# Performance work log

Measured on AMD Instinct MI355X. Metric: run time of the kernel, lower is better.

The kernel has to match this reference:

```python
import jax, jax.numpy as jnp
import numpy as np

K = 15  # window_size


def setup_inputs() -> dict:
    key = jax.random.key(0)
    k1, k2, k3, k4 = jax.random.split(key, 4)
    x = jax.random.normal(k1, (8, 256, 240, 240), dtype=jnp.float32)
    wq = jax.random.normal(k2, (144, 256), dtype=jnp.float32) * (1.0 / np.sqrt(256))
    wk = jax.random.normal(k3, (144, 256), dtype=jnp.float32) * (1.0 / np.sqrt(256))
    wproj = jax.random.normal(k4, (256, 256), dtype=jnp.float32) * (1.0 / np.sqrt(256))
    return {"x": x, "wq": wq, "wk": wk, "wproj": wproj}


def _pnlm(x, wq, wk, wproj):
    b, c, h, w = x.shape
    ph, pw = (-h) % K, (-w) % K
    if ph or pw:
        x_pad = jnp.pad(x, ((0, 0), (0, 0), (0, ph), (0, pw)), mode='reflect')
    else:
        x_pad = x
    H, W = x_pad.shape[2], x_pad.shape[3]
    nh, nw = H // K, W // K
    N = K * K  # tokens per window
    # blockify: (B,C,H,W) -> (B*nh*nw, C, N)
    blocks = (x_pad.reshape(b, c, nh, K, nw, K)
              .transpose(0, 2, 4, 1, 3, 5)
              .reshape(b * nh * nw, c, N))
    q = jnp.einsum('ec,bcn->bne', wq, blocks)   # (B', N, E)
    km = jnp.einsum('ec,bcm->bem', wk, blocks)  # (B', E, N)
    att = jnp.einsum('bne,bem->bnm', q, km)     # (B', N, N)
    scale = 1.0 / jnp.sqrt(jnp.asarray(q.shape[-1], dtype=att.dtype))
    att = jax.nn.softmax(att * scale, axis=-1)
    y = jnp.einsum('bnm,bcm->bcn', att, blocks)  # att @ V, V = blocks^T
    y = jnp.einsum('oc,bcn->bon', wproj, y)      # 1x1 proj_out
    # unblockify: (B', C, N) -> (B, C, H, W)
    y = (y.reshape(b, nh, nw, c, K, K)
         .transpose(0, 3, 1, 4, 2, 5)
         .reshape(b, c, H, W))
    y = y[:, :, :h, :w]
    return x + y


def reference(x, wq, wk, wproj):
    return _pnlm(x, wq, wk, wproj)
```

## Files before the change

### kernel.cpp

```cpp
#include <hip/hip_runtime.h>


typedef __bf16 bf16x8 __attribute__((ext_vector_type(8)));
typedef float  f32x4  __attribute__((ext_vector_type(4)));

#define MFMA(a,b,c) __builtin_amdgcn_mfma_f32_16x16x32_bf16((a),(b),(c),0,0,0)

#define QK_ROW 320
#define KL_STRIDE 168
#define XBB_ROW 240

__device__ __forceinline__ unsigned short f2bf(float f){
  union { float f; unsigned int u; } v; v.f = f;
  unsigned int r = v.u + 0x7FFFu + ((v.u >> 16) & 1u);
  return (unsigned short)(r >> 16);
}
__device__ __forceinline__ float bf2f(unsigned short u){
  union { unsigned int u; float f; } v; v.u = ((unsigned int)u) << 16;
  return v.f;
}
__device__ __forceinline__ int swz(int row, int col){
  return row*256 + ((((col >> 3) ^ (row & 7)) << 3) | (col & 7));
}
__device__ __forceinline__ int swzC(int row, int col){
  return row*256 + (col ^ ((((row >> 3) ^ row) & 7) << 3));
}
__device__ __forceinline__ bf16x8 ld_frag_lds(const unsigned short* p, int idx){
  uint4 v = *(const uint4*)(p + idx);
  return __builtin_bit_cast(bf16x8, v);
}
__device__ __forceinline__ bf16x8 ld_frag_b(const void* p){
  uint4 v = *(const uint4*)(p);
  return __builtin_bit_cast(bf16x8, v);
}

__device__ __forceinline__ void repack_frag(const unsigned int* plo, const unsigned int* phi,
                                            uint4* outf, int lane){
  const int nn = lane & 15, hh = lane >> 4;
  const int sla = nn + 32*(hh & 1);
  const int slb = sla + 16;
  const bool up = hh >= 2;
  #pragma unroll
  for (int k = 0; k < 8; ++k){
    unsigned int a0 = (unsigned int)__shfl((int)plo[2*k],   sla);
    unsigned int a1 = (unsigned int)__shfl((int)plo[2*k+1], sla);
    unsigned int b0 = (unsigned int)__shfl((int)phi[2*k],   sla);
    unsigned int b1 = (unsigned int)__shfl((int)phi[2*k+1], sla);
    unsigned int c0 = (unsigned int)__shfl((int)plo[2*k],   slb);
    unsigned int c1 = (unsigned int)__shfl((int)plo[2*k+1], slb);
    unsigned int d0 = (unsigned int)__shfl((int)phi[2*k],   slb);
    unsigned int d1 = (unsigned int)__shfl((int)phi[2*k+1], slb);
    outf[k] = make_uint4(up?a1:a0, up?b1:b0, up?c1:c0, up?d1:d0);
  }
}

__global__ __launch_bounds__(256) void k_w(
    const float* __restrict__ wq, const float* __restrict__ wk,
    const float* __restrict__ wproj,
    unsigned short* __restrict__ wqb, unsigned short* __restrict__ wkb,
    unsigned short* __restrict__ wpb)
{
  int i = blockIdx.x*256 + threadIdx.x;
  if (i < 20480){
    int e = i >> 7, c = (i & 127)*2;
    unsigned int v = 0;
    if (e < 144) v = (unsigned int)f2bf(wq[e*256+c]) | ((unsigned int)f2bf(wq[e*256+c+1]) << 16);
    *(unsigned int*)(wqb + (size_t)i*2) = v;
  } else if (i < 40960){
    int j = i - 20480;
    int e = j >> 7, c = (j & 127)*2;
    unsigned int v = 0;
    if (e < 144) v = (unsigned int)f2bf(wk[e*256+c]) | ((unsigned int)f2bf(wk[e*256+c+1]) << 16);
    *(unsigned int*)(wkb + (size_t)j*2) = v;
  } else if (i < 73728){
    int l = i - 40960;
    int o = l >> 7, c = (l & 127)*2;
    *(unsigned int*)(wpb + (size_t)l*2) =
        (unsigned int)f2bf(wproj[o*256+c]) | ((unsigned int)f2bf(wproj[o*256+c+1]) << 16);
  }
}

__global__ __launch_bounds__(256) void k_xb(
    const float* __restrict__ x, unsigned short* __restrict__ xbb)
{
  __shared__ unsigned short xs[8*15*240];
  const int wg = blockIdx.x;
  const int cg = wg & 31;
  const int th = (wg >> 5) & 15;
  const int b  = wg >> 9;
  const int tid = threadIdx.x;

  const float* xb = x + ((size_t)b*256 + cg*8)*57600 + th*15*240;
  for (int i = tid; i < 8*15*120; i += 256){
    int c = i / 1800;
    int rem = i - c*1800;
    int r = rem / 120, p2 = rem - r*120;
    float2 v = *(const float2*)(xb + (size_t)c*57600 + r*240 + p2*2);
    *(unsigned int*)(&xs[(c*15 + r)*240 + p2*2]) =
        (unsigned int)f2bf(v.x) | ((unsigned int)f2bf(v.y) << 16);
  }
  __syncthreads();

  for (int i = tid; i < 8*16*30; i += 256){
    int c = i / 480;
    int rem = i - c*480;
    int tw = rem / 30, ch = rem - tw*30;
    union { unsigned short u16[8]; uint4 u4; } pk;
    #pragma unroll
    for (int j = 0; j < 8; ++j){
      int m = ch*8 + j;
      int r = m / 15, s = m - r*15;
      pk.u16[j] = (m <= 224) ? xs[(c*15 + r)*240 + tw*15 + s] : (unsigned short)0;
    }
    *(uint4*)(xbb + ((size_t)(b*256 + th*16 + tw)*256 + cg*8 + c)*XBB_ROW + ch*8) = pk.u4;
  }
}

__global__ __launch_bounds__(512) void k_qkb(
    const unsigned short* __restrict__ xbb,
    const unsigned short* __restrict__ wqb, const unsigned short* __restrict__ wkb,
    unsigned short* __restrict__ qkws)
{
  __shared__ __align__(16) unsigned short S[32768];
  unsigned short* xt  = S;
  unsigned short* wqs = S;
  unsigned short* wks = S + 8192;
  const int wg = blockIdx.x;
  const int b  = wg >> 8;
  const int th = (wg >> 4) & 15, tw = wg & 15;
  const int h0 = th*15, w0 = tw*15;
  const int tid = threadIdx.x;
  const int lane = tid & 63, wave = tid >> 6;
  const int col  = lane & 15, hi = lane >> 4;
  const unsigned short* xbw = xbb + (size_t)wg * (256*XBB_ROW);

  bf16x8 af[2][8];
  #pragma unroll 1
  for (int half = 0; half < 2; ++half){
    if (half) __syncthreads();
    for (int i = tid; i < 256*16; i += 512){
      int c = i >> 4, m8 = i & 15;
      int m = half*128 + m8*8;
      if (m + 8 <= 240){
        uint4 v = *(const uint4*)(xbw + (size_t)c*XBB_ROW + m);
        const unsigned short* pv = (const unsigned short*)&v;
        #pragma unroll
        for (int j = 0; j < 8; ++j)
          xt[swzC(m8*8 + j, c)] = pv[j];
      }
    }
    __syncthreads();
    const int rloc = wave*16 + col;
    if (half == 0){
      #pragma unroll
      for (int k = 0; k < 8; ++k)
        af[0][k] = ld_frag_lds(xt, swzC(rloc, k*32 + hi*8));
    } else {
      #pragma unroll
      for (int k = 0; k < 8; ++k)
        af[1][k] = ld_frag_lds(xt, swzC(rloc, k*32 + hi*8));
    }
  }
  __syncthreads();

  #pragma unroll 1
  for (int eg = 0; eg < 5; ++eg){
    if (eg) __syncthreads();
    for (int i = tid; i < 32*32; i += 512){
      int e_l = i >> 5, c8 = (i & 31)*8;
      size_t off = (size_t)(eg*32 + e_l)*256 + c8;
      *(uint4*)(&wqs[swz(e_l, c8)]) = *(const uint4*)(wqb + off);
      *(uint4*)(&wks[swz(e_l, c8)]) = *(const uint4*)(wkb + off);
    }
    __syncthreads();
    #pragma unroll
    for (int h2 = 0; h2 < 2; ++h2){
      const int t = h2*8 + wave;
      if (t < 15){
        #pragma unroll
        for (int et = 0; et < 2; ++et){
          f32x4 aq = {0.f,0.f,0.f,0.f}, ak = {0.f,0.f,0.f,0.f};
          const int el = et*16 + col;
          #pragma unroll
          for (int k = 0; k < 8; ++k){
            int idx = swz(el, k*32 + hi*8);
            bf16x8 bq = ld_frag_lds(wqs, idx);
            bf16x8 bk = ld_frag_lds(wks, idx);
            aq = MFMA(af[h2][k], bq, aq);
            ak = MFMA(af[h2][k], bk, ak);
          }
          const int e_out = eg*32 + et*16 + col;
          #pragma unroll
          for (int jj = 0; jj < 4; ++jj){
            int m_px = t*16 + hi*4 + jj;
            if (m_px <= 224){
              int hw = (h0 + m_px/15)*240 + w0 + m_px%15;
              size_t row = ((size_t)b*57600 + hw)*QK_ROW;
              qkws[row + e_out]       = f2bf(aq[jj]);
              qkws[row + 160 + e_out] = f2bf(ak[jj]);
            }
          }
        }
      }
    }
  }
}

__global__ __launch_bounds__(512,4) void k_attn_b(
    const unsigned short* __restrict__ xbb, const unsigned short* __restrict__ wpb,
    const unsigned short* __restrict__ qkws, float* __restrict__ out)
{
  __shared__ __align__(16) unsigned short S[40960];
  unsigned short* kl = S;
  unsigned short* xl = S;
  unsigned short* wl = S + 32768;
  unsigned int*  hwp = (unsigned int*)(S + 40320);
  const int wg = blockIdx.x;
  const int b  = wg >> 8;
  const int th = (wg >> 4) & 15, tw = wg & 15;
  const int h0 = th*15, w0 = tw*15;
  const int tid = threadIdx.x;
  const int lane = tid & 63, wave = tid >> 6;
  const int col  = lane & 15, hi = lane >> 4;
  const size_t obase = (size_t)b * 256 * 57600;
  const unsigned short* qkb = qkws + (size_t)b * 57600 * QK_ROW;
  const unsigned short* xbw = xbb + (size_t)wg * (256*XBB_ROW);

  if (tid < 240){
    int ms = tid <= 224 ? tid : 224;
    hwp[tid] = (unsigned int)((h0 + ms/15)*240 + w0 + ms%15);
  }
  __syncthreads();

  for (int i = tid; i < 240*20; i += 512){
    int m = i / 20, eb = i - m*20;
    *(uint4*)(&kl[m*KL_STRIDE + eb*8]) =
        *(const uint4*)(qkb + (size_t)hwp[m]*QK_ROW + 160 + eb*8);
  }
  __syncthreads();

  uint4 attf[2][8];
  #pragma unroll
  for (int slot = 0; slot < 2; ++slot){
    const int nt = wave + slot*8;
    if (nt < 15){
      const int n  = nt*16 + col;
      const int na = n <= 224 ? n : 224;
      const unsigned short* qrow = qkb + (size_t)hwp[na]*QK_ROW;
      bf16x8 qf[5];
      #pragma unroll
      for (int c = 0; c < 5; ++c)
        qf[c] = ld_frag_b(qrow + c*32 + hi*8);
      f32x4 at[15];
      #pragma unroll
      for (int T = 0; T < 15; ++T){
        f32x4 acc = {0.f,0.f,0.f,0.f};
        #pragma unroll
        for (int c = 0; c < 5; ++c){
          bf16x8 kf = ld_frag_lds(kl, (T*16 + col)*KL_STRIDE + c*32 + hi*8);
          acc = MFMA(kf, qf[c], acc);
        }
        at[T] = acc;
      }
      const float sc = 0.12022458674074695f;
      float M = -3.0e38f;
      #pragma unroll
      for (int T = 0; T < 15; ++T){
        #pragma unroll
        for (int jj = 0; jj < 4; ++jj){
          int m = T*16 + hi*4 + jj;
          if (m <= 224) M = fmaxf(M, at[T][jj]*sc);
        }
      }
      M = fmaxf(M, __shfl_xor(M, 16));
      M = fmaxf(M, __shfl_xor(M, 32));
      float Ssum = 0.f;
      #pragma unroll
      for (int T = 0; T < 15; ++T){
        #pragma unroll
        for (int jj = 0; jj < 4; ++jj){
          int m = T*16 + hi*4 + jj;
          float v = (m <= 224) ? exp2f(at[T][jj]*sc - M) : 0.f;
          at[T][jj] = v; Ssum += v;
        }
      }
      Ssum += __shfl_xor(Ssum, 16);
      Ssum += __shfl_xor(Ssum, 32);
      const float inv = 1.0f / Ssum;
      unsigned int plo[16], phi[16];
      #pragma unroll
      for (int T = 0; T < 15; ++T){
        plo[T] = (unsigned int)f2bf(at[T][0]*inv) | ((unsigned int)f2bf(at[T][1]*inv) << 16);
        phi[T] = (unsigned int)f2bf(at[T][2]*inv) | ((unsigned int)f2bf(at[T][3]*inv) << 16);
      }
      plo[15] = 0u; phi[15] = 0u;
      repack_frag(plo, phi, attf[slot], lane);
    }
  }

  int pixs[2];
  #pragma unroll
  for (int slot = 0; slot < 2; ++slot){
    const int n = (wave + slot*8)*16 + col;
    pixs[slot] = (n <= 224) ? (int)hwp[n] : -1;
  }

  unsigned int ylo[2][16], yhi[2][16];
  #pragma unroll
  for (int half = 0; half < 2; ++half){
    __syncthreads();
    for (int i = tid; i < 128*32; i += 512){
      int c = i >> 5, m8 = i & 31;
      uint4 v = make_uint4(0u,0u,0u,0u);
      if (m8 < 30)
        v = *(const uint4*)(xbw + (size_t)(half*128 + c)*XBB_ROW + m8*8);
      *(uint4*)(&xl[swz(c, m8*8)]) = v;
    }
    __syncthreads();
    #pragma unroll
    for (int slot = 0; slot < 2; ++slot){
      const int nt = wave + slot*8;
      if (nt < 15){
        #pragma unroll
        for (int ct = 0; ct < 8; ++ct){
          f32x4 acc = {0.f,0.f,0.f,0.f};
          #pragma unroll
          for (int k = 0; k < 8; ++k){
            bf16x8 xf = ld_frag_lds(xl, swz(ct*16 + col, k*32 + hi*8));
            acc = MFMA(xf, __builtin_bit_cast(bf16x8, attf[slot][k]), acc);
          }
          ylo[slot][half*8 + ct] = (unsigned int)f2bf(acc[0]) | ((unsigned int)f2bf(acc[1]) << 16);
          yhi[slot][half*8 + ct] = (unsigned int)f2bf(acc[2]) | ((unsigned int)f2bf(acc[3]) << 16);
        }
      }
    }
  }

  uint4 y1f[2][8];
  #pragma unroll
  for (int slot = 0; slot < 2; ++slot){
    const int nt = wave + slot*8;
    if (nt < 15)
      repack_frag(ylo[slot], yhi[slot], y1f[slot], lane);
  }

  #pragma unroll 1
  for (int oe = 0; oe < 8; ++oe){
    __syncthreads();
    for (int i = tid; i < 32*32; i += 512){
      int olr = i >> 5, c8 = (i & 31)*8;
      *(uint4*)(&wl[swz(olr, c8)]) =
          *(const uint4*)(wpb + (size_t)(oe*32 + olr)*256 + c8);
    }
    __syncthreads();
    #pragma unroll
    for (int ot = 0; ot < 2; ++ot){
      bf16x8 awf[8];
      const int olr = ot*16 + col;
      #pragma unroll
      for (int k = 0; k < 8; ++k)
        awf[k] = ld_frag_lds(wl, swz(olr, k*32 + hi*8));
      #pragma unroll
      for (int slot = 0; slot < 2; ++slot){
        const int nt = wave + slot*8;
        if (nt < 15){
          f32x4 y2 = {0.f,0.f,0.f,0.f};
          #pragma unroll
          for (int k = 0; k < 8; ++k)
            y2 = MFMA(awf[k], __builtin_bit_cast(bf16x8, y1f[slot][k]), y2);
          const int n = nt*16 + col;
          if (n <= 224){
            const size_t pix = (size_t)pixs[slot];
            #pragma unroll
            for (int jj = 0; jj < 4; ++jj){
              int o = oe*32 + ot*16 + hi*4 + jj;
              float xr = bf2f(xbw[(size_t)o*XBB_ROW + n]);
              out[obase + (size_t)o*57600 + pix] = y2[jj] + xr;
            }
          }
        }
      }
    }
  }
}

__global__ __launch_bounds__(512) void k_qk(
    const float* __restrict__ x, const float* __restrict__ wq,
    const float* __restrict__ wk,
    unsigned short* __restrict__ qkws)
{
  __shared__ __align__(16) unsigned short S[32768];
  unsigned short* xt  = S;
  unsigned short* wqs = S;
  unsigned short* wks = S + 8192;
  const int wg  = blockIdx.x;
  const int b   = wg / 450;
  const int hw0 = (wg % 450) * 128;
  const int tid = threadIdx.x;
  const int lane = tid & 63, wave = tid >> 6;
  const int col  = lane & 15, hi = lane >> 4;

  {
    const float* xb = x + (size_t)b * 256 * 57600 + hw0;
    const int hw_l = tid & 127;
    #pragma unroll 4
    for (int i = 0; i < 32; ++i){
      int c = ((tid >> 7) * 32 + i) * 2;
      float f0 = xb[(size_t)c     * 57600 + hw_l];
      float f1 = xb[(size_t)(c+1) * 57600 + hw_l];
      *(unsigned int*)(&xt[swz(hw_l, c)]) =
          (unsigned int)f2bf(f0) | ((unsigned int)f2bf(f1) << 16);
    }
  }
  __syncthreads();

  bf16x8 af[8];
  const int arow = wave*16 + col;
  #pragma unroll
  for (int k = 0; k < 8; ++k)
    af[k] = ld_frag_lds(xt, swz(arow, k*32 + hi*8));

  const size_t orow_base = (size_t)b*57600 + hw0 + wave*16;

  for (int eg = 0; eg < 5; ++eg){
    __syncthreads();
    for (int i = 0; i < 8; ++i){
      int idx = tid + i*512;
      int e_l = idx >> 7, c = (idx & 127) * 2;
      int e = eg*32 + e_l;
      float2 vq = make_float2(0.f,0.f), vk = make_float2(0.f,0.f);
      if (e < 144){
        vq = *(const float2*)(wq + (size_t)e*256 + c);
        vk = *(const float2*)(wk + (size_t)e*256 + c);
      }
      *(unsigned int*)(&wqs[swz(e_l, c)]) =
          (unsigned int)f2bf(vq.x) | ((unsigned int)f2bf(vq.y) << 16);
      *(unsigned int*)(&wks[swz(e_l, c)]) =
          (unsigned int)f2bf(vk.x) | ((unsigned int)f2bf(vk.y) << 16);
    }
    __syncthreads();
    #pragma unroll
    for (int etl = 0; etl < 2; ++etl){
      f32x4 aq = {0.f,0.f,0.f,0.f}, ak = {0.f,0.f,0.f,0.f};
      const int el = etl*16 + col;
      #pragma unroll
      for (int k = 0; k < 8; ++k){
        int idx = swz(el, k*32 + hi*8);
        bf16x8 bq = ld_frag_lds(wqs, idx);
        bf16x8 bk = ld_frag_lds(wks, idx);
        aq = MFMA(af[k], bq, aq);
        ak = MFMA(af[k], bk, ak);
      }
      const int e_out = eg*32 + etl*16 + col;
      #pragma unroll
      for (int jj = 0; jj < 4; ++jj){
        size_t row = orow_base + hi*4 + jj;
        qkws[row*QK_ROW + e_out]       = f2bf(aq[jj]);
        qkws[row*QK_ROW + 160 + e_out] = f2bf(ak[jj]);
      }
    }
  }
}

__global__ __launch_bounds__(512,4) void k_attn_s(
    const float* __restrict__ x, const float* __restrict__ wproj,
    const unsigned short* __restrict__ qkws, float* __restrict__ out)
{
  __shared__ __align__(16) unsigned short S[40320 + 480];
  unsigned short* kl = S;
  unsigned short* xl = S;
  unsigned short* wl = S + 32768;
  unsigned int*  hwp = (unsigned int*)(S + 40320);
  const int wg = blockIdx.x;
  const int b  = wg >> 8;
  const int th = (wg >> 4) & 15, tw = wg & 15;
  const int h0 = th*15, w0 = tw*15;
  const int tid = threadIdx.x;
  const int lane = tid & 63, wave = tid >> 6;
  const int col  = lane & 15, hi = lane >> 4;
  const size_t xbase = (size_t)b * 256 * 57600;
  const unsigned short* qkb = qkws + (size_t)b * 57600 * QK_ROW;

  if (tid < 240){
    int ms = tid <= 224 ? tid : 224;
    hwp[tid] = (unsigned int)((h0 + ms/15)*240 + w0 + ms%15);
  }
  __syncthreads();

  for (int i = tid; i < 240*20; i += 512){
    int m = i / 20, eb = i - m*20;
    *(uint4*)(&kl[m*KL_STRIDE + eb*8]) =
        *(const uint4*)(qkb + (size_t)hwp[m]*QK_ROW + 160 + eb*8);
  }
  __syncthreads();

  uint4 attf[2][8];
  #pragma unroll
  for (int slot = 0; slot < 2; ++slot){
    const int nt = wave + slot*8;
    if (nt < 15){
      const int n  = nt*16 + col;
      const int na = n <= 224 ? n : 224;
      const unsigned short* qrow = qkb + (size_t)hwp[na]*QK_ROW;
      bf16x8 qf[5];
      #pragma unroll
      for (int c = 0; c < 5; ++c)
        qf[c] = ld_frag_b(qrow + c*32 + hi*8);
      f32x4 at[15];
      #pragma unroll
      for (int T = 0; T < 15; ++T){
        f32x4 acc = {0.f,0.f,0.f,0.f};
        #pragma unroll
        for (int c = 0; c < 5; ++c){
          bf16x8 kf = ld_frag_lds(kl, (T*16 + col)*KL_STRIDE + c*32 + hi*8);
          acc = MFMA(kf, qf[c], acc);
        }
        at[T] = acc;
      }
      const float sc = 0.12022458674074695f;
      float M = -3.0e38f;
      #pragma unroll
      for (int T = 0; T < 15; ++T){
        #pragma unroll
        for (int jj = 0; jj < 4; ++jj){
          int m = T*16 + hi*4 + jj;
          if (m <= 224) M = fmaxf(M, at[T][jj]*sc);
        }
      }
      M = fmaxf(M, __shfl_xor(M, 16));
      M = fmaxf(M, __shfl_xor(M, 32));
      float Ssum = 0.f;
      #pragma unroll
      for (int T = 0; T < 15; ++T){
        #pragma unroll
        for (int jj = 0; jj < 4; ++jj){
          int m = T*16 + hi*4 + jj;
          float v = (m <= 224) ? exp2f(at[T][jj]*sc - M) : 0.f;
          at[T][jj] = v; Ssum += v;
        }
      }
      Ssum += __shfl_xor(Ssum, 16);
      Ssum += __shfl_xor(Ssum, 32);
      const float inv = 1.0f / Ssum;
      unsigned int plo[16], phi[16];
      #pragma unroll
      for (int T = 0; T < 15; ++T){
        plo[T] = (unsigned int)f2bf(at[T][0]*inv) | ((unsigned int)f2bf(at[T][1]*inv) << 16);
        phi[T] = (unsigned int)f2bf(at[T][2]*inv) | ((unsigned int)f2bf(at[T][3]*inv) << 16);
      }
      plo[15] = 0u; phi[15] = 0u;
      repack_frag(plo, phi, attf[slot], lane);
    }
  }

  unsigned int ylo[2][16], yhi[2][16];
  #pragma unroll
  for (int half = 0; half < 2; ++half){
    __syncthreads();
    for (int i = tid; i < 128*128; i += 512){
      int c = i >> 7, m = (i & 127)*2;
      int m0 = m <= 224 ? m : 224;
      float f0 = (m     <= 224) ? x[xbase + (size_t)(half*128 + c)*57600 + hwp[m0]]   : 0.f;
      float f1 = (m + 1 <= 224) ? x[xbase + (size_t)(half*128 + c)*57600 + hwp[m0+1]] : 0.f;
      *(unsigned int*)(&xl[swz(c, m)]) =
          (unsigned int)f2bf(f0) | ((unsigned int)f2bf(f1) << 16);
    }
    __syncthreads();
    #pragma unroll
    for (int slot = 0; slot < 2; ++slot){
      const int nt = wave + slot*8;
      if (nt < 15){
        #pragma unroll
        for (int ct = 0; ct < 8; ++ct){
          f32x4 acc = {0.f,0.f,0.f,0.f};
          #pragma unroll
          for (int k = 0; k < 8; ++k){
            bf16x8 xf = ld_frag_lds(xl, swz(ct*16 + col, k*32 + hi*8));
            acc = MFMA(xf, __builtin_bit_cast(bf16x8, attf[slot][k]), acc);
          }
          ylo[slot][half*8 + ct] = (unsigned int)f2bf(acc[0]) | ((unsigned int)f2bf(acc[1]) << 16);
          yhi[slot][half*8 + ct] = (unsigned int)f2bf(acc[2]) | ((unsigned int)f2bf(acc[3]) << 16);
        }
      }
    }
  }

  uint4 y1f[2][8];
  #pragma unroll
  for (int slot = 0; slot < 2; ++slot){
    const int nt = wave + slot*8;
    if (nt < 15)
      repack_frag(ylo[slot], yhi[slot], y1f[slot], lane);
  }

  #pragma unroll 1
  for (int oe = 0; oe < 16; ++oe){
    __syncthreads();
    for (int i = tid; i < 16*128; i += 512){
      int olr = i >> 7, c = (i & 127)*2;
      const float* wr = wproj + (size_t)(oe*16 + olr)*256 + c;
      *(unsigned int*)(&wl[swz(olr, c)]) =
          (unsigned int)f2bf(wr[0]) | ((unsigned int)f2bf(wr[1]) << 16);
    }
    __syncthreads();
    bf16x8 awf[8];
    #pragma unroll
    for (int k = 0; k < 8; ++k)
      awf[k] = ld_frag_lds(wl, swz(col, k*32 + hi*8));
    #pragma unroll
    for (int slot = 0; slot < 2; ++slot){
      const int nt = wave + slot*8;
      if (nt < 15){
        f32x4 y2 = {0.f,0.f,0.f,0.f};
        #pragma unroll
        for (int k = 0; k < 8; ++k)
          y2 = MFMA(awf[k], __builtin_bit_cast(bf16x8, y1f[slot][k]), y2);
        const int n = nt*16 + col;
        if (n <= 224){
          const size_t pix = hwp[n];
          #pragma unroll
          for (int jj = 0; jj < 4; ++jj){
            int o = oe*16 + hi*4 + jj;
            const size_t idx = xbase + (size_t)o*57600 + pix;
            out[idx] = y2[jj] + x[idx];
          }
        }
      }
    }
  }
}

extern "C" void kernel_launch(void* const* d_in, const int* in_sizes, int n_in,
                              void* d_out, int out_size, void* d_ws, size_t ws_size,
                              hipStream_t stream)
{
  const float* x     = (const float*)d_in[0];
  const float* wq    = (const float*)d_in[1];
  const float* wk    = (const float*)d_in[2];
  const float* wproj = (const float*)d_in[3];
  float* out = (float*)d_out;
  (void)in_sizes; (void)n_in; (void)out_size;

  const size_t QKWS_B = (size_t)8*57600*QK_ROW*2;
  const size_t XBB_B  = (size_t)8*256*256*XBB_ROW*2;
  const size_t WB_ALL = (size_t)(160*256 + 160*256 + 256*256)*2;
  unsigned short* qkws = (unsigned short*)d_ws;

  if (ws_size >= QKWS_B + XBB_B + WB_ALL){
    unsigned short* xbb = (unsigned short*)((char*)d_ws + QKWS_B);
    unsigned short* wqb = (unsigned short*)((char*)d_ws + QKWS_B + XBB_B);
    unsigned short* wkb = wqb + 160*256;
    unsigned short* wpb = wkb + 160*256;
    k_w     <<<dim3(288),  dim3(256), 0, stream>>>(wq, wk, wproj, wqb, wkb, wpb);
    k_xb    <<<dim3(4096), dim3(256), 0, stream>>>(x, xbb);
    k_qkb   <<<dim3(2048), dim3(512), 0, stream>>>(xbb, wqb, wkb, qkws);
    k_attn_b<<<dim3(2048), dim3(512), 0, stream>>>(xbb, wpb, qkws, out);
  } else {
    k_qk    <<<dim3(3600), dim3(512), 0, stream>>>(x, wq, wk, qkws);
    k_attn_s<<<dim3(2048), dim3(512), 0, stream>>>(x, wproj, qkws, out);
  }
}
```

Baseline: 954.5 us.

## Fuse QK projection and windowed attention kernels into one launch

Merges the Q/K projection kernel and the attention+projection kernel into a single kernel, so each workgroup computes its window's Q/K and then immediately runs attention on it. Intermediate Q/K still goes through global memory, but it is read back by the same workgroup while likely still in L2, and one launch plus its tail are removed. The output projection loop now stages 64 weight rows per iteration instead of 32, halving the barriers. Risk: the stricter launch bounds applied to the QK phase may increase register pressure or spills.

Result: no change. 945.7 us, median of 2 (-0.9%).

```diff
diff --git a/kernel.cpp b/kernel.cpp
--- a/kernel.cpp
+++ b/kernel.cpp
@@ -116,15 +116,20 @@
   }
 }
 
-__global__ __launch_bounds__(512) void k_qkb(
+__global__ __launch_bounds__(512,4) void k_fused(
     const unsigned short* __restrict__ xbb,
     const unsigned short* __restrict__ wqb, const unsigned short* __restrict__ wkb,
-    unsigned short* __restrict__ qkws)
+    const unsigned short* __restrict__ wpb,
+    unsigned short* __restrict__ qkws, float* __restrict__ out)
 {
-  __shared__ __align__(16) unsigned short S[32768];
+  __shared__ __align__(16) unsigned short S[40960];
   unsigned short* xt  = S;
   unsigned short* wqs = S;
   unsigned short* wks = S + 8192;
+  unsigned short* kl  = S;
+  unsigned short* xl  = S;
+  unsigned short* wl  = S;
+  unsigned int*  hwp  = (unsigned int*)(S + 40320);
   const int wg = blockIdx.x;
   const int b  = wg >> 8;
   const int th = (wg >> 4) & 15, tw = wg & 15;
@@ -132,7 +137,14 @@
   const int tid = threadIdx.x;
   const int lane = tid & 63, wave = tid >> 6;
   const int col  = lane & 15, hi = lane >> 4;
+  const size_t obase = (size_t)b * 256 * 57600;
+  const unsigned short* qkb = qkws + (size_t)b * 57600 * QK_ROW;
   const unsigned short* xbw = xbb + (size_t)wg * (256*XBB_ROW);
+
+  if (tid < 240){
+    int ms = tid <= 224 ? tid : 224;
+    hwp[tid] = (unsigned int)((h0 + ms/15)*240 + w0 + ms%15);
+  }
 
   bf16x8 af[2][8];
   #pragma unroll 1
@@ -204,32 +216,6 @@
       }
     }
   }
-}
-
-__global__ __launch_bounds__(512,4) void k_attn_b(
-    const unsigned short* __restrict__ xbb, const unsigned short* __restrict__ wpb,
-    const unsigned short* __restrict__ qkws, float* __restrict__ out)
-{
-  __shared__ __align__(16) unsigned short S[40960];
-  unsigned short* kl = S;
-  unsigned short* xl = S;
-  unsigned short* wl = S + 32768;
-  unsigned int*  hwp = (unsigned int*)(S + 40320);
-  const int wg = blockIdx.x;
-  const int b  = wg >> 8;
-  const int th = (wg >> 4) & 15, tw = wg & 15;
-  const int h0 = th*15, w0 = tw*15;
-  const int tid = threadIdx.x;
-  const int lane = tid & 63, wave = tid >> 6;
-  const int col  = lane & 15, hi = lane >> 4;
-  const size_t obase = (size_t)b * 256 * 57600;
-  const unsigned short* qkb = qkws + (size_t)b * 57600 * QK_ROW;
-  const unsigned short* xbw = xbb + (size_t)wg * (256*XBB_ROW);
-
-  if (tid < 240){
-    int ms = tid <= 224 ? tid : 224;
-    hwp[tid] = (unsigned int)((h0 + ms/15)*240 + w0 + ms%15);
-  }
   __syncthreads();
 
   for (int i = tid; i < 240*20; i += 512){
@@ -345,16 +331,16 @@
   }
 
   #pragma unroll 1
-  for (int oe = 0; oe < 8; ++oe){
-    __syncthreads();
-    for (int i = tid; i < 32*32; i += 512){
+  for (int oe2 = 0; oe2 < 4; ++oe2){
+    __syncthreads();
+    for (int i = tid; i < 64*32; i += 512){
       int olr = i >> 5, c8 = (i & 31)*8;
       *(uint4*)(&wl[swz(olr, c8)]) =
-          *(const uint4*)(wpb + (size_t)(oe*32 + olr)*256 + c8);
-    }
-    __syncthreads();
-    #pragma unroll
-    for (int ot = 0; ot < 2; ++ot){
+          *(const uint4*)(wpb + (size_t)(oe2*64 + olr)*256 + c8);
+    }
+    __syncthreads();
+    #pragma unroll
+    for (int ot = 0; ot < 4; ++ot){
       bf16x8 awf[8];
       const int olr = ot*16 + col;
       #pragma unroll
@@ -373,7 +359,7 @@
             const size_t pix = (size_t)pixs[slot];
             #pragma unroll
             for (int jj = 0; jj < 4; ++jj){
-              int o = oe*32 + ot*16 + hi*4 + jj;
+              int o = oe2*64 + ot*16 + hi*4 + jj;
               float xr = bf2f(xbw[(size_t)o*XBB_ROW + n]);
               out[obase + (size_t)o*57600 + pix] = y2[jj] + xr;
             }
@@ -651,10 +637,9 @@
     unsigned short* wqb = (unsigned short*)((char*)d_ws + QKWS_B + XBB_B);
     unsigned short* wkb = wqb + 160*256;
     unsigned short* wpb = wkb + 160*256;
-    k_w     <<<dim3(288),  dim3(256), 0, stream>>>(wq, wk, wproj, wqb, wkb, wpb);
-    k_xb    <<<dim3(4096), dim3(256), 0, stream>>>(x, xbb);
-    k_qkb   <<<dim3(2048), dim3(512), 0, stream>>>(xbb, wqb, wkb, qkws);
-    k_attn_b<<<dim3(2048), dim3(512), 0, stream>>>(xbb, wpb, qkws, out);
+    k_w    <<<dim3(288),  dim3(256), 0, stream>>>(wq, wk, wproj, wqb, wkb, wpb);
+    k_xb   <<<dim3(4096), dim3(256), 0, stream>>>(x, xbb);
+    k_fused<<<dim3(2048), dim3(512), 0, stream>>>(xbb, wqb, wkb, wpb, qkws, out);
   } else {
     k_qk    <<<dim3(3600), dim3(512), 0, stream>>>(x, wq, wk, qkws);
     k_attn_s<<<dim3(2048), dim3(512), 0, stream>>>(x, wproj, qkws, out);
```
